# Kernel optimization log

Measured on AMD Instinct MI355X. Metric: run time of the kernel, lower is better.

The kernel has to match this reference:

```python
import jax, jax.numpy as jnp
import numpy as np

N_FILTRATIONS = 24
TEMPERATURE = 0.15
H1_WEIGHT = 0.5
LAMBDA_TOPO = 0.1


def setup_inputs() -> dict:
    key = jax.random.key(0)
    embeddings = jax.random.normal(key, (4096, 512), dtype=jnp.float32)
    return {"embeddings": embeddings, "step": 0}


def _landscape_loss(embeddings):
    N = embeddings.shape[0]
    emb = embeddings.astype(jnp.float32)
    # pairwise euclidean distances (torch.cdist p=2), safe sqrt for grad at 0
    sq = jnp.sum(emb * emb, axis=1)
    d2 = sq[:, None] + sq[None, :] - 2.0 * (emb @ emb.T)
    d2 = jnp.maximum(d2, 0.0)
    pos = d2 > 1e-12
    dist = jnp.where(pos, jnp.sqrt(jnp.where(pos, d2, 1.0)), 0.0)
    eye = jnp.eye(N, dtype=jnp.float32)
    dist = dist + eye * 1e9  # [N, N], diag pushed to 'infinity'
    off = dist < 1e8
    # thresholds come from .item() in torch -> no grad through them
    d_min = jax.lax.stop_gradient(jnp.min(jnp.where(off, dist, jnp.inf)))
    d_max = jax.lax.stop_gradient(
        jnp.maximum(jnp.max(jnp.where(off, dist, -jnp.inf)), d_min + 1e-4))
    thresholds = jnp.linspace(d_min, d_max, N_FILTRATIONS)

    one_minus_eye = 1.0 - eye

    def step_fn(carry, thresh):
        adj = jax.nn.sigmoid((thresh - dist) / TEMPERATURE) * one_minus_eye
        deg = jnp.clip(jnp.sum(adj, axis=-1), 1e-6, None)
        n_isolated = jnp.sum((deg < 0.5).astype(jnp.float32))  # H0 proxy
        n_edges_soft = jnp.sum(adj) / 2.0
        n_excess = jax.nn.relu(n_edges_soft - (N - 1)) / N  # H1 proxy
        return carry, (n_isolated, n_excess)

    _, (h0, h1) = jax.lax.scan(step_fn, None, thresholds)
    h0_loss = jnp.mean(h0[-8:])
    h1_loss = jnp.mean(h1)
    total = h0_loss + H1_WEIGHT * h1_loss
    return total * LAMBDA_TOPO


def reference(embeddings, step) -> jnp.ndarray:
    # warmup_steps = 0, so the warmup skip branch never triggers;
    # N == max_points, so no subsampling.
    return _landscape_loss(embeddings)
```

## Files before the change

### kernel.cpp

```cpp
#include <hip/hip_runtime.h>
#include <stdint.h>

typedef float f32x4 __attribute__((ext_vector_type(4)));
typedef short s16x8 __attribute__((ext_vector_type(8)));
typedef unsigned short us4 __attribute__((ext_vector_type(4)));

#define NPTS 4096
#define DDIM 512
#define NF   24
#define NBLK 32
#define NB   2048

#define OFF_SQ  4194304
#define OFF_MM  4210688
#define OFF_DEG 4210752
#define OFF_D   4603968
#define OFF_H   38158400ULL
#define WS_A    54935616ULL

typedef __attribute__((address_space(1))) void gvoid;
typedef __attribute__((address_space(3))) void svoid;
#define GLD16(gp, lp) __builtin_amdgcn_global_load_lds((gvoid*)(gp), (svoid*)(lp), 16, 0, 0)

static __device__ __forceinline__ ushort f2h(float x) {
    _Float16 h = (_Float16)x;
    return __builtin_bit_cast(unsigned short, h);
}
static __device__ __forceinline__ float h2f(ushort u) {
    return (float)__builtin_bit_cast(_Float16, u);
}

__global__ __launch_bounds__(256) void k_init(float* __restrict__ deg,
                                              unsigned* __restrict__ mm) {
    int i = blockIdx.x * 256 + threadIdx.x;
    if (i < NPTS * NF) deg[i] = 0.0f;
    if (i == 0) { mm[0] = 0x7F7FFFFFu; mm[1] = 0u; }
}

__global__ __launch_bounds__(256) void k_convert(const float* __restrict__ in,
                                                 ushort* __restrict__ Eb,
                                                 float* __restrict__ sq,
                                                 float* __restrict__ acc32,
                                                 unsigned* __restrict__ mm) {
    if (blockIdx.x == 0) {
        if (threadIdx.x < 32) acc32[threadIdx.x] = 0.0f;
        else if (threadIdx.x == 32) mm[0] = 0x7F7FFFFFu;
        else if (threadIdx.x == 33) mm[1] = 0u;
    }
    const int w = threadIdx.x >> 6, lane = threadIdx.x & 63;
    const int row = blockIdx.x * 4 + w;
    const float* src = in + (size_t)row * DDIM + lane * 8;
    float4 a = ((const float4*)src)[0];
    float4 b = ((const float4*)src)[1];
    float v[8] = {a.x, a.y, a.z, a.w, b.x, b.y, b.z, b.w};
    unsigned u[8];
    float ss = 0.0f;
#pragma unroll
    for (int i = 0; i < 8; ++i) {
        ss += v[i] * v[i];
        unsigned bits = __float_as_uint(v[i]);
        u[i] = (bits + 0x7FFFu + ((bits >> 16) & 1u)) >> 16;
    }
    uint4 pk;
    pk.x = u[0] | (u[1] << 16);
    pk.y = u[2] | (u[3] << 16);
    pk.z = u[4] | (u[5] << 16);
    pk.w = u[6] | (u[7] << 16);
    *(uint4*)(Eb + (size_t)row * DDIM + lane * 8) = pk;
#pragma unroll
    for (int s = 1; s < 64; s <<= 1) ss += __shfl_xor(ss, s);
    if (lane == 0) sq[row] = ss;
}

__global__ __launch_bounds__(256) void k_gram_v3u(const ushort* __restrict__ Eb,
                                                  const float* __restrict__ sq,
                                                  unsigned* __restrict__ mm,
                                                  ushort* __restrict__ D2h) {
    __shared__ __align__(16) ushort SM[17408];
    __shared__ float sqr[128], sqc[128], red[8];
    char* SMb = (char*)SM;
    const int tid = threadIdx.x;
    const int w = tid >> 6, lane = tid & 63, g = lane >> 4, l15 = lane & 15;
    const int wr = w >> 1, wc = w & 1;

    int bid = blockIdx.x, rb = 0, pre = 0;
    while (pre + (NBLK - rb) <= bid) { pre += NBLK - rb; ++rb; }
    const int cb = rb + (bid - pre);

    if (tid < 128) sqr[tid] = sq[rb * 128 + tid];
    else           sqc[tid - 128] = sq[cb * 128 + (tid - 128)];

    f32x4 acc[4][4];
#pragma unroll
    for (int i = 0; i < 4; ++i)
#pragma unroll
        for (int j = 0; j < 4; ++j) acc[i][j] = (f32x4){0.f, 0.f, 0.f, 0.f};

    const int lrow = lane >> 2, lch = lane & 3;

#define STAGE(buf, kk)                                                          \
    {                                                                           \
        const int k0_ = (kk) * 32;                                              \
        _Pragma("unroll")                                                       \
        for (int i_ = 0; i_ < 2; ++i_) {                                        \
            const int r_  = w * 32 + i_ * 16 + lrow;                            \
            const int ch_ = lch ^ ((r_ >> 1) & 3);                              \
            GLD16(Eb + (size_t)(rb * 128 + r_) * DDIM + k0_ + ch_ * 8,          \
                  SMb + (buf) * 8192 + (w * 32 + i_ * 16) * 64);                \
            GLD16(Eb + (size_t)(cb * 128 + r_) * DDIM + k0_ + ch_ * 8,          \
                  SMb + 16384 + (buf) * 8192 + (w * 32 + i_ * 16) * 64);        \
        }                                                                       \
    }

    STAGE(0, 0);
    int cur = 0;
#pragma unroll 1
    for (int kk = 0; kk < 16; ++kk) {
        __syncthreads();
        if (kk < 15) STAGE(cur ^ 1, kk + 1);
        s16x8 rf[4], cf[4];
#pragma unroll
        for (int i = 0; i < 4; ++i) {
            const int r = wr * 64 + i * 16 + l15;
            rf[i] = *(const s16x8*)(SMb + cur * 8192 + r * 64 + ((g ^ ((r >> 1) & 3)) * 16));
        }
#pragma unroll
        for (int j = 0; j < 4; ++j) {
            const int r = wc * 64 + j * 16 + l15;
            cf[j] = *(const s16x8*)(SMb + 16384 + cur * 8192 + r * 64 + ((g ^ ((r >> 1) & 3)) * 16));
        }
#pragma unroll
        for (int i = 0; i < 4; ++i)
#pragma unroll
            for (int j = 0; j < 4; ++j)
                acc[i][j] = __builtin_amdgcn_mfma_f32_16x16x32_bf16(cf[j], rf[i], acc[i][j], 0, 0, 0);
        cur ^= 1;
    }
    __syncthreads();

    ushort* T = SM;
    float mn = 3.4e38f, mx = 0.0f;
#pragma unroll
    for (int i = 0; i < 4; ++i) {
        const int lr = wr * 64 + i * 16 + l15;
        const int trow = rb * 128 + lr;
        const float srv = sqr[lr];
#pragma unroll
        for (int j = 0; j < 4; ++j) {
            const int c0 = wc * 64 + j * 16 + g * 4;
            const int tc0 = cb * 128 + c0;
            ushort h[4];
#pragma unroll
            for (int m = 0; m < 4; ++m) {
                float d2 = srv + sqc[c0 + m] - 2.0f * acc[i][j][m];
                d2 = fmaxf(d2, 0.0f);
                bool diag = (tc0 + m == trow);
                mn = diag ? mn : fminf(mn, d2);
                mx = diag ? mx : fmaxf(mx, d2);
                h[m] = f2h(diag ? 6.0e4f : d2);
            }
            us4 pk4 = {h[0], h[1], h[2], h[3]};
            *(us4*)(T + lr * 136 + c0) = pk4;
        }
    }
#pragma unroll
    for (int s = 1; s < 64; s <<= 1) {
        mn = fminf(mn, __shfl_xor(mn, s));
        mx = fmaxf(mx, __shfl_xor(mx, s));
    }
    if (lane == 0) { red[w] = mn; red[4 + w] = mx; }
    __syncthreads();
    if (tid == 0) {
        mn = fminf(fminf(red[0], red[1]), fminf(red[2], red[3]));
        mx = fmaxf(fmaxf(red[4], red[5]), fmaxf(red[6], red[7]));
        atomicMin(&mm[0], __float_as_uint(mn));
        atomicMax(&mm[1], __float_as_uint(mx));
    }
#pragma unroll
    for (int j = 0; j < 8; ++j) {
        const int c = j * 256 + tid;
        const int row = c >> 4, col8 = (c & 15) * 8;
        uint4 v = *(const uint4*)(T + row * 136 + col8);
        *(uint4*)(D2h + (size_t)(rb * 128 + row) * NPTS + cb * 128 + col8) = v;
    }
    if (rb != cb) {
        __syncthreads();
#pragma unroll
        for (int i = 0; i < 4; ++i) {
            const int lr = wr * 64 + i * 16 + l15;
            const float srv = sqr[lr];
#pragma unroll
            for (int j = 0; j < 4; ++j) {
                const int c0 = wc * 64 + j * 16 + g * 4;
#pragma unroll
                for (int m = 0; m < 4; ++m) {
                    float d2 = srv + sqc[c0 + m] - 2.0f * acc[i][j][m];
                    d2 = fmaxf(d2, 0.0f);
                    T[(c0 + m) * 136 + lr] = f2h(d2);
                }
            }
        }
        __syncthreads();
#pragma unroll
        for (int j2 = 0; j2 < 8; ++j2) {
            const int c = j2 * 256 + tid;
            const int row = c >> 4, col8 = (c & 15) * 8;
            uint4 v = *(const uint4*)(T + row * 136 + col8);
            *(uint4*)(D2h + (size_t)(cb * 128 + row) * NPTS + rb * 128 + col8) = v;
        }
    }
}

__global__ __launch_bounds__(256) void k_hist4(const ushort* __restrict__ D2h,
                                               const unsigned* __restrict__ mm,
                                               ushort* __restrict__ H) {
    __shared__ unsigned Hs[4][NB + 4];
    const int tid = threadIdx.x, w = tid >> 6, lane = tid & 63;
    const int row0 = blockIdx.x * 4;
    const int row = row0 + w;
    for (int i = tid; i < 4 * (NB + 4); i += 256) ((unsigned*)Hs)[i] = 0u;
    const float d2min = __uint_as_float(mm[0]);
    const float d2max = __uint_as_float(mm[1]);
    const float sc = (float)NB / fmaxf(d2max - d2min, 1e-6f);
    __syncthreads();
    const uint4* Dv = (const uint4*)(D2h + (size_t)row * NPTS);
    unsigned* hr = Hs[w];
#pragma unroll
    for (int it = 0; it < 8; ++it) {
        uint4 pk = Dv[it * 64 + lane];
        unsigned pw[4] = {pk.x, pk.y, pk.z, pk.w};
#pragma unroll
        for (int i = 0; i < 4; ++i) {
            float a = h2f((ushort)(pw[i] & 0xFFFFu));
            float b = h2f((ushort)(pw[i] >> 16));
            if (a < 3.0e4f) {
                int ba = (int)fminf(fmaxf((a - d2min) * sc, 0.0f), (float)(NB - 1));
                atomicAdd(&hr[ba], 1u);
            }
            if (b < 3.0e4f) {
                int bb = (int)fminf(fmaxf((b - d2min) * sc, 0.0f), (float)(NB - 1));
                atomicAdd(&hr[bb], 1u);
            }
        }
    }
    __syncthreads();
    unsigned* Ho = (unsigned*)(H + (size_t)row0 * NB);
    for (int i = tid; i < 4 * (NB / 2); i += 256) {
        const int r = i >> 10, pw_ = i & 1023;
        unsigned lo = Hs[r][2 * pw_], hi = Hs[r][2 * pw_ + 1];
        Ho[r * (NB / 2) + pw_] = (lo & 0xFFFFu) | (hi << 16);
    }
}

__global__ __launch_bounds__(512) void k_dot(const ushort* __restrict__ H,
                                             const unsigned* __restrict__ mm,
                                             float* __restrict__ acc32) {
    __shared__ float Wl[4][NB];
    __shared__ float degb[8][NF];
    const int tid = threadIdx.x;
    const int wid = tid >> 6, lane = tid & 63;
    const int row = blockIdx.x * 8 + wid;

    const float d2min = __uint_as_float(mm[0]);
    const float d2max = __uint_as_float(mm[1]);
    const float bw    = fmaxf(d2max - d2min, 1e-6f) / (float)NB;
    const float d_min = d2min > 1e-12f ? sqrtf(d2min) : 0.0f;
    const float d_mx  = d2max > 1e-12f ? sqrtf(d2max) : 0.0f;
    const float d_max = fmaxf(d_mx, d_min + 1e-4f);
    const float stp   = (d_max - d_min) / 23.0f;
    const float S2L   = (1.0f / 0.15f) * 1.44269504f;
    const float Ds2   = stp * S2L;
    const float R     = exp2f(-Ds2);
    const float LIM   = 1073741824.0f;

    float hv[32];
    const ushort* Hr = H + (size_t)row * NB;
#pragma unroll
    for (int j = 0; j < 8; ++j) {
        uint2 pk = *(const uint2*)(Hr + j * 256 + lane * 4);
        hv[j * 4 + 0] = (float)(pk.x & 0xFFFFu);
        hv[j * 4 + 1] = (float)(pk.x >> 16);
        hv[j * 4 + 2] = (float)(pk.y & 0xFFFFu);
        hv[j * 4 + 3] = (float)(pk.y >> 16);
    }

    float e4[4];
#pragma unroll
    for (int q = 0; q < 4; ++q) {
        const int b = tid * 4 + q;
        const float d2c = d2min + ((float)b + 0.5f) * bw;
        const float db = sqrtf(fmaxf(d2c, 0.0f));
        e4[q] = exp2f(fminf((db - d_min) * S2L, 125.0f));
    }

#pragma unroll 1
    for (int ph = 0; ph < 6; ++ph) {
        __syncthreads();
#pragma unroll
        for (int k = 0; k < 4; ++k) {
            f32x4 sg;
#pragma unroll
            for (int q = 0; q < 4; ++q) {
                sg[q] = __builtin_amdgcn_rcpf(1.0f + fminf(e4[q], LIM));
                e4[q] *= R;
            }
            *(f32x4*)(&Wl[k][tid * 4]) = sg;
        }
        __syncthreads();
        float dacc[4];
#pragma unroll
        for (int k = 0; k < 4; ++k) {
            const float* Wr = &Wl[k][0];
            float s = 0.0f;
#pragma unroll
            for (int j = 0; j < 8; ++j) {
                const f32x4 wv = *(const f32x4*)(Wr + j * 256 + lane * 4);
                s += hv[j*4+0]*wv[0] + hv[j*4+1]*wv[1] + hv[j*4+2]*wv[2] + hv[j*4+3]*wv[3];
            }
            dacc[k] = s;
        }
#pragma unroll
        for (int k = 0; k < 4; ++k)
#pragma unroll
            for (int o = 1; o < 64; o <<= 1) dacc[k] += __shfl_xor(dacc[k], o);
        if (lane == 0) {
#pragma unroll
            for (int k = 0; k < 4; ++k) degb[wid][ph * 4 + k] = dacc[k];
        }
    }
    __syncthreads();
    if (tid < NF) {
        float s = 0.0f;
#pragma unroll
        for (int r = 0; r < 8; ++r) s += degb[r][tid];
        atomicAdd(&acc32[tid], s);
    } else if (tid < 32) {
        const int k = 16 + (tid - NF);
        float c = 0.0f;
#pragma unroll
        for (int r = 0; r < 8; ++r) c += (degb[r][k] < 0.5f) ? 1.0f : 0.0f;
        atomicAdd(&acc32[tid], c);
    }
}

__global__ __launch_bounds__(64) void k_final2(const float* __restrict__ acc32,
                                               float* __restrict__ out) {
    if (threadIdx.x == 0) {
        float h1 = 0.0f;
#pragma unroll
        for (int k = 0; k < NF; ++k)
            h1 += fmaxf(acc32[k] * 0.5f - (float)(NPTS - 1), 0.0f) * (1.0f / (float)NPTS);
        float h0 = 0.0f;
#pragma unroll
        for (int k = 0; k < 8; ++k) h0 += acc32[NF + k];
        out[0] = (h0 * 0.125f + 0.5f * (h1 * (1.0f / 24.0f))) * 0.1f;
    }
}

__device__ __forceinline__ void gram_tile(const ushort* __restrict__ Eb, int rb, int cb,
                                          ushort* As, ushort* Bs, f32x4 acc[2][8]) {
    const int tid = threadIdx.x;
    const int w = tid >> 6, lane = tid & 63, g = lane >> 4, l15 = lane & 15;
#pragma unroll 1
    for (int kk = 0; kk < DDIM / 32; ++kk) {
        const int k0 = kk * 32;
        __syncthreads();
#pragma unroll
        for (int it = 0; it < 2; ++it) {
            int li  = it * 256 + tid;
            int row = li >> 2, ch = li & 3;
            uint4 va = *(const uint4*)(Eb + (size_t)(rb * 128 + row) * DDIM + k0 + ch * 8);
            uint4 vb = *(const uint4*)(Eb + (size_t)(cb * 128 + row) * DDIM + k0 + ch * 8);
            *(uint4*)(As + row * 32 + ch * 8) = va;
            *(uint4*)(Bs + row * 32 + ch * 8) = vb;
        }
        __syncthreads();
        s16x8 rf0 = *(const s16x8*)(As + (w * 32 + 0 * 16 + l15) * 32 + g * 8);
        s16x8 rf1 = *(const s16x8*)(As + (w * 32 + 1 * 16 + l15) * 32 + g * 8);
#pragma unroll
        for (int bj = 0; bj < 8; ++bj) {
            s16x8 cf = *(const s16x8*)(Bs + (bj * 16 + l15) * 32 + g * 8);
            acc[0][bj] = __builtin_amdgcn_mfma_f32_16x16x32_bf16(cf, rf0, acc[0][bj], 0, 0, 0);
            acc[1][bj] = __builtin_amdgcn_mfma_f32_16x16x32_bf16(cf, rf1, acc[1][bj], 0, 0, 0);
        }
    }
}

__global__ __launch_bounds__(256) void k_minmax(const ushort* __restrict__ Eb,
                                                const float* __restrict__ sq,
                                                unsigned* __restrict__ mm) {
    const int rb = blockIdx.y, cb = blockIdx.x;
    if (cb < rb) return;
    __shared__ ushort As[128 * 32], Bs[128 * 32];
    __shared__ float sqr[128], sqc[128];
    __shared__ float red[8];
    const int tid = threadIdx.x;
    if (tid < 128) sqr[tid] = sq[rb * 128 + tid];
    else           sqc[tid - 128] = sq[cb * 128 + (tid - 128)];
    f32x4 acc[2][8];
#pragma unroll
    for (int bi = 0; bi < 2; ++bi)
#pragma unroll
        for (int bj = 0; bj < 8; ++bj) acc[bi][bj] = (f32x4){0.f, 0.f, 0.f, 0.f};
    gram_tile(Eb, rb, cb, As, Bs, acc);
    const int w = tid >> 6, lane = tid & 63, g = lane >> 4, l15 = lane & 15;
    const float sr0 = sqr[w * 32 + l15], sr1 = sqr[w * 32 + 16 + l15];
    float mn = 3.4e38f, mx = 0.0f;
#pragma unroll
    for (int bi = 0; bi < 2; ++bi)
#pragma unroll
        for (int bj = 0; bj < 8; ++bj)
#pragma unroll
            for (int m = 0; m < 4; ++m) {
                int tr = w * 32 + bi * 16 + l15;
                int tc = bj * 16 + g * 4 + m;
                float d2 = (bi ? sr1 : sr0) + sqc[tc] - 2.0f * acc[bi][bj][m];
                d2 = fmaxf(d2, 0.0f);
                bool diag = (rb == cb) && (tr == tc);
                mn = diag ? mn : fminf(mn, d2);
                mx = diag ? mx : fmaxf(mx, d2);
            }
#pragma unroll
    for (int s = 1; s < 64; s <<= 1) {
        mn = fminf(mn, __shfl_xor(mn, s));
        mx = fmaxf(mx, __shfl_xor(mx, s));
    }
    if (lane == 0) { red[w] = mn; red[4 + w] = mx; }
    __syncthreads();
    if (tid == 0) {
        mn = fminf(fminf(red[0], red[1]), fminf(red[2], red[3]));
        mx = fmaxf(fmaxf(red[4], red[5]), fmaxf(red[6], red[7]));
        atomicMin(&mm[0], __float_as_uint(mn));
        atomicMax(&mm[1], __float_as_uint(mx));
    }
}

__global__ __launch_bounds__(256) void k_accum2(const ushort* __restrict__ Eb,
                                                const float* __restrict__ sq,
                                                const unsigned* __restrict__ mm,
                                                float* __restrict__ deg) {
    const int rb = blockIdx.y, cb = blockIdx.x;
    __shared__ ushort As[128 * 32], Bs[128 * 32];
    __shared__ float sqr[128], sqc[128];
    __shared__ float degr[128][NF];
    const int tid = threadIdx.x;
    if (tid < 128) sqr[tid] = sq[rb * 128 + tid];
    else           sqc[tid - 128] = sq[cb * 128 + (tid - 128)];
    for (int i = tid; i < 128 * NF; i += 256) ((float*)degr)[i] = 0.0f;
    f32x4 acc[2][8];
#pragma unroll
    for (int bi = 0; bi < 2; ++bi)
#pragma unroll
        for (int bj = 0; bj < 8; ++bj) acc[bi][bj] = (f32x4){0.f, 0.f, 0.f, 0.f};
    gram_tile(Eb, rb, cb, As, Bs, acc);
    const int w = tid >> 6, lane = tid & 63, g = lane >> 4, l15 = lane & 15;

    const float dmin2 = __uint_as_float(mm[0]);
    const float dmax2 = __uint_as_float(mm[1]);
    const float d_min = dmin2 > 1e-12f ? sqrtf(dmin2) : 0.0f;
    const float d_mx  = dmax2 > 1e-12f ? sqrtf(dmax2) : 0.0f;
    const float d_max = fmaxf(d_mx, d_min + 1e-4f);
    const float stp   = (d_max - d_min) / 23.0f;
    const float S2L   = (1.0f / 0.15f) * 1.44269504f;
    const float Ds2   = stp * S2L;
    const float R     = exp2f(-Ds2);
    const float LIM   = 1073741824.0f;
    const float ECAP  = 125.0f;

    const float sr0 = sqr[w * 32 + l15], sr1 = sqr[w * 32 + 16 + l15];
    f32x4 ee[2][8];
#pragma unroll
    for (int bi = 0; bi < 2; ++bi)
#pragma unroll
        for (int bj = 0; bj < 8; ++bj)
#pragma unroll
            for (int m = 0; m < 4; ++m) {
                int tr = w * 32 + bi * 16 + l15;
                int tc = bj * 16 + g * 4 + m;
                float d2 = (bi ? sr1 : sr0) + sqc[tc] - 2.0f * acc[bi][bj][m];
                d2 = fmaxf(d2, 0.0f);
                float d = d2 > 1e-12f ? sqrtf(d2) : 0.0f;
                if (rb == cb && tr == tc) d = 1e9f;
                ee[bi][bj][m] = exp2f(fminf((d - d_min) * S2L, ECAP));
            }

#pragma unroll 1
    for (int t = 0; t < NF; ++t) {
        float rs0 = 0.0f, rs1 = 0.0f;
#pragma unroll
        for (int bj = 0; bj < 8; ++bj) {
            {
                f32x4 q = ee[0][bj];
                float A  = 1.0f + fminf(q.x, LIM), B  = 1.0f + fminf(q.y, LIM);
                float Cq = 1.0f + fminf(q.z, LIM), Dq = 1.0f + fminf(q.w, LIM);
                float sAB = A + B,  sCD = Cq + Dq;
                float pAB = A * B,  pCD = Cq * Dq;
                rs0 += (sAB * pCD + sCD * pAB) * __builtin_amdgcn_rcpf(pAB * pCD);
                ee[0][bj] = q * R;
            }
            {
                f32x4 q = ee[1][bj];
                float A  = 1.0f + fminf(q.x, LIM), B  = 1.0f + fminf(q.y, LIM);
                float Cq = 1.0f + fminf(q.z, LIM), Dq = 1.0f + fminf(q.w, LIM);
                float sAB = A + B,  sCD = Cq + Dq;
                float pAB = A * B,  pCD = Cq * Dq;
                rs1 += (sAB * pCD + sCD * pAB) * __builtin_amdgcn_rcpf(pAB * pCD);
                ee[1][bj] = q * R;
            }
        }
        rs0 += __shfl_xor(rs0, 16); rs0 += __shfl_xor(rs0, 32);
        rs1 += __shfl_xor(rs1, 16); rs1 += __shfl_xor(rs1, 32);
        if (g == 0) {
            degr[w * 32 + l15][t]      += rs0;
            degr[w * 32 + 16 + l15][t] += rs1;
        }
    }
    __syncthreads();
    for (int i = tid; i < 128 * NF; i += 256) {
        int r = i / NF, t = i % NF;
        atomicAdd(&deg[(size_t)(rb * 128 + r) * NF + t], degr[r][t]);
    }
}

__global__ __launch_bounds__(256) void k_final(const float* __restrict__ deg,
                                               float* __restrict__ out) {
    const int tid = threadIdx.x;
    float s[NF], cnt[8];
#pragma unroll
    for (int t = 0; t < NF; ++t) s[t] = 0.0f;
#pragma unroll
    for (int k = 0; k < 8; ++k) cnt[k] = 0.0f;
    for (int i = tid; i < NPTS; i += 256) {
        const float* row = deg + (size_t)i * NF;
#pragma unroll
        for (int t = 0; t < NF; ++t) {
            float v = row[t];
            s[t] += v;
            if (t >= 16) cnt[t - 16] += (v < 0.5f) ? 1.0f : 0.0f;
        }
    }
#pragma unroll
    for (int t = 0; t < NF; ++t)
#pragma unroll
        for (int o = 1; o < 64; o <<= 1) s[t] += __shfl_xor(s[t], o);
#pragma unroll
    for (int k = 0; k < 8; ++k)
#pragma unroll
        for (int o = 1; o < 64; o <<= 1) cnt[k] += __shfl_xor(cnt[k], o);
    __shared__ float red[4][32];
    const int w = tid >> 6, lane = tid & 63;
    if (lane == 0) {
#pragma unroll
        for (int t = 0; t < NF; ++t) red[w][t] = s[t];
#pragma unroll
        for (int k = 0; k < 8; ++k) red[w][NF + k] = cnt[k];
    }
    __syncthreads();
    if (tid == 0) {
        float h0 = 0.0f, h1 = 0.0f;
#pragma unroll
        for (int t = 0; t < NF; ++t) {
            float S = red[0][t] + red[1][t] + red[2][t] + red[3][t];
            float edges = S * 0.5f;
            h1 += fmaxf(edges - (float)(NPTS - 1), 0.0f) / (float)NPTS;
        }
#pragma unroll
        for (int k = 0; k < 8; ++k)
            h0 += red[0][NF + k] + red[1][NF + k] + red[2][NF + k] + red[3][NF + k];
        h0 *= (1.0f / 8.0f);
        h1 *= (1.0f / 24.0f);
        out[0] = (h0 + 0.5f * h1) * 0.1f;
    }
}

extern "C" void kernel_launch(void* const* d_in, const int* in_sizes, int n_in,
                              void* d_out, int out_size, void* d_ws, size_t ws_size,
                              hipStream_t stream) {
    (void)in_sizes; (void)n_in; (void)out_size;
    const float* emb = (const float*)d_in[0];
    uint8_t* ws = (uint8_t*)d_ws;
    ushort*   Eb  = (ushort*)(ws);
    float*    sqv = (float*)(ws + OFF_SQ);
    unsigned* mm  = (unsigned*)(ws + OFF_MM);
    float*    deg = (float*)(ws + OFF_DEG);
    ushort*   D2h = (ushort*)(ws + OFF_D);
    ushort*   H   = (ushort*)(ws + OFF_H);
    float*    out = (float*)d_out;
    const bool bigws = (ws_size >= WS_A);

    if (bigws) {
        k_convert <<<dim3(NPTS / 4),              dim3(256), 0, stream>>>(emb, Eb, sqv, deg, mm);
        k_gram_v3u<<<dim3(NBLK * (NBLK + 1) / 2), dim3(256), 0, stream>>>(Eb, sqv, mm, D2h);
        k_hist4   <<<dim3(NPTS / 4),              dim3(256), 0, stream>>>(D2h, mm, H);
        k_dot     <<<dim3(NPTS / 8),              dim3(512), 0, stream>>>(H, mm, deg);
        k_final2  <<<dim3(1),                     dim3(64),  0, stream>>>(deg, out);
    } else {
        k_init   <<<dim3(384),      dim3(256), 0, stream>>>(deg, mm);
        k_convert<<<dim3(NPTS / 4), dim3(256), 0, stream>>>(emb, Eb, sqv, deg, mm);
        k_minmax <<<dim3(32, 32),   dim3(256), 0, stream>>>(Eb, sqv, mm);
        k_accum2 <<<dim3(32, 32),   dim3(256), 0, stream>>>(Eb, sqv, mm, deg);
        k_final  <<<dim3(1),        dim3(256), 0, stream>>>(deg, out);
    }
}
```

Before: 85.48 us.

## Triple-buffer gram kernel LDS stages with explicit vmcnt waits

Replaces the double-buffered K loop in the bf16 gram kernel with a three-stage LDS ring buffer. Two tiles are prefetched ahead, and precise s_waitcnt vmcnt counts let loads stay in flight across iterations instead of draining at every barrier. This hides more global-load latency behind the MFMA work. In exchange it uses more shared memory per block, which may lower occupancy, and the hand-counted waits must match the number of issued loads.

```diff
diff --git a/kernel.cpp b/kernel.cpp
--- a/kernel.cpp
+++ b/kernel.cpp
@@ -76,7 +76,7 @@
                                                   const float* __restrict__ sq,
                                                   unsigned* __restrict__ mm,
                                                   ushort* __restrict__ D2h) {
-    __shared__ __align__(16) ushort SM[17408];
+    __shared__ __align__(16) ushort SM[24576];
     __shared__ float sqr[128], sqc[128], red[8];
     char* SMb = (char*)SM;
     const int tid = threadIdx.x;
@@ -108,34 +108,50 @@
             GLD16(Eb + (size_t)(rb * 128 + r_) * DDIM + k0_ + ch_ * 8,          \
                   SMb + (buf) * 8192 + (w * 32 + i_ * 16) * 64);                \
             GLD16(Eb + (size_t)(cb * 128 + r_) * DDIM + k0_ + ch_ * 8,          \
-                  SMb + 16384 + (buf) * 8192 + (w * 32 + i_ * 16) * 64);        \
+                  SMb + 24576 + (buf) * 8192 + (w * 32 + i_ * 16) * 64);        \
         }                                                                       \
     }
 
+#define KSTEP(WAITN, kk, DOSTAGE)                                               \
+    {                                                                           \
+        asm volatile("s_waitcnt vmcnt(" #WAITN ")" ::: "memory");               \
+        __builtin_amdgcn_s_barrier();                                           \
+        __builtin_amdgcn_sched_barrier(0);                                      \
+        const char* Ac = SMb + bcur * 8192;                                     \
+        const char* Bc = SMb + 24576 + bcur * 8192;                             \
+        s16x8 rf[4], cf[4];                                                     \
+        _Pragma("unroll")                                                       \
+        for (int i = 0; i < 4; ++i) {                                           \
+            const int r = wr * 64 + i * 16 + l15;                               \
+            rf[i] = *(const s16x8*)(Ac + r * 64 + ((g ^ ((r >> 1) & 3)) * 16)); \
+        }                                                                       \
+        _Pragma("unroll")                                                       \
+        for (int j = 0; j < 4; ++j) {                                           \
+            const int r = wc * 64 + j * 16 + l15;                               \
+            cf[j] = *(const s16x8*)(Bc + r * 64 + ((g ^ ((r >> 1) & 3)) * 16)); \
+        }                                                                       \
+        _Pragma("unroll")                                                       \
+        for (int i = 0; i < 4; ++i)                                             \
+            _Pragma("unroll")                                                   \
+            for (int j = 0; j < 4; ++j)                                         \
+                acc[i][j] = __builtin_amdgcn_mfma_f32_16x16x32_bf16(            \
+                    cf[j], rf[i], acc[i][j], 0, 0, 0);                          \
+        asm volatile("s_waitcnt lgkmcnt(0)" ::: "memory");                      \
+        __builtin_amdgcn_s_barrier();                                           \
+        __builtin_amdgcn_sched_barrier(0);                                      \
+        if (DOSTAGE) { STAGE(bcur, (kk) + 3); }                                 \
+        bcur = (bcur == 2) ? 0 : bcur + 1;                                      \
+    }
+
     STAGE(0, 0);
-    int cur = 0;
+    STAGE(1, 1);
+    STAGE(2, 2);
+    int bcur = 0;
 #pragma unroll 1
-    for (int kk = 0; kk < 16; ++kk) {
-        __syncthreads();
-        if (kk < 15) STAGE(cur ^ 1, kk + 1);
-        s16x8 rf[4], cf[4];
-#pragma unroll
-        for (int i = 0; i < 4; ++i) {
-            const int r = wr * 64 + i * 16 + l15;
-            rf[i] = *(const s16x8*)(SMb + cur * 8192 + r * 64 + ((g ^ ((r >> 1) & 3)) * 16));
-        }
-#pragma unroll
-        for (int j = 0; j < 4; ++j) {
-            const int r = wc * 64 + j * 16 + l15;
-            cf[j] = *(const s16x8*)(SMb + 16384 + cur * 8192 + r * 64 + ((g ^ ((r >> 1) & 3)) * 16));
-        }
-#pragma unroll
-        for (int i = 0; i < 4; ++i)
-#pragma unroll
-            for (int j = 0; j < 4; ++j)
-                acc[i][j] = __builtin_amdgcn_mfma_f32_16x16x32_bf16(cf[j], rf[i], acc[i][j], 0, 0, 0);
-        cur ^= 1;
-    }
+    for (int kk = 0; kk < 13; ++kk) KSTEP(8, kk, 1);
+    KSTEP(8, 13, 0);
+    KSTEP(4, 14, 0);
+    KSTEP(0, 15, 0);
     __syncthreads();
 
     ushort* T = SM;
```

Measured after the change: 89.37 us. +4.5%, slower.

## Deepen Gram GEMM K-tile to 64 and remap block order for XCD locality

Applied to the files above, without the earlier changes.

The Gram kernel now stages 64-wide K slices instead of 32, halving the number of loop iterations and barriers. It uses a 128-byte-row LDS layout with an XOR-8 swizzle and does two MFMA sub-steps per stage. It also permutes block IDs so that consecutive triangle tiles go to the same XCD (stride 8, 66 blocks each), aiming for better L2 reuse of row panels. LDS use doubles to 64KB plus extras, which may lower occupancy per CU.

```diff
diff --git a/kernel.cpp b/kernel.cpp
--- a/kernel.cpp
+++ b/kernel.cpp
@@ -72,18 +72,19 @@
     if (lane == 0) sq[row] = ss;
 }
 
-__global__ __launch_bounds__(256) void k_gram_v3u(const ushort* __restrict__ Eb,
-                                                  const float* __restrict__ sq,
-                                                  unsigned* __restrict__ mm,
-                                                  ushort* __restrict__ D2h) {
-    __shared__ __align__(16) ushort SM[17408];
+__global__ __launch_bounds__(256) void k_gram_bk64(const ushort* __restrict__ Eb,
+                                                   const float* __restrict__ sq,
+                                                   unsigned* __restrict__ mm,
+                                                   ushort* __restrict__ D2h) {
+    __shared__ __align__(16) ushort SM[32768];
     __shared__ float sqr[128], sqc[128], red[8];
     char* SMb = (char*)SM;
     const int tid = threadIdx.x;
     const int w = tid >> 6, lane = tid & 63, g = lane >> 4, l15 = lane & 15;
     const int wr = w >> 1, wc = w & 1;
 
-    int bid = blockIdx.x, rb = 0, pre = 0;
+    int bid = (blockIdx.x & 7) * 66 + (blockIdx.x >> 3);
+    int rb = 0, pre = 0;
     while (pre + (NBLK - rb) <= bid) { pre += NBLK - rb; ++rb; }
     const int cb = rb + (bid - pre);
 
@@ -96,44 +97,52 @@
 #pragma unroll
         for (int j = 0; j < 4; ++j) acc[i][j] = (f32x4){0.f, 0.f, 0.f, 0.f};
 
-    const int lrow = lane >> 2, lch = lane & 3;
-
-#define STAGE(buf, kk)                                                          \
+    const int srow_off = lane >> 3, slch = lane & 7;
+
+#define STAGE64(buf, kk)                                                        \
     {                                                                           \
-        const int k0_ = (kk) * 32;                                              \
+        const int k0_ = (kk) * 64;                                              \
         _Pragma("unroll")                                                       \
-        for (int i_ = 0; i_ < 2; ++i_) {                                        \
-            const int r_  = w * 32 + i_ * 16 + lrow;                            \
-            const int ch_ = lch ^ ((r_ >> 1) & 3);                              \
+        for (int i_ = 0; i_ < 4; ++i_) {                                        \
+            const int r_  = w * 32 + i_ * 8 + srow_off;                         \
+            const int ch_ = slch ^ (r_ & 7);                                    \
             GLD16(Eb + (size_t)(rb * 128 + r_) * DDIM + k0_ + ch_ * 8,          \
-                  SMb + (buf) * 8192 + (w * 32 + i_ * 16) * 64);                \
+                  SMb + (buf) * 16384 + (w * 32 + i_ * 8) * 128);               \
             GLD16(Eb + (size_t)(cb * 128 + r_) * DDIM + k0_ + ch_ * 8,          \
-                  SMb + 16384 + (buf) * 8192 + (w * 32 + i_ * 16) * 64);        \
+                  SMb + 32768 + (buf) * 16384 + (w * 32 + i_ * 8) * 128);       \
         }                                                                       \
     }
 
-    STAGE(0, 0);
+    STAGE64(0, 0);
     int cur = 0;
 #pragma unroll 1
-    for (int kk = 0; kk < 16; ++kk) {
+    for (int kk = 0; kk < 8; ++kk) {
         __syncthreads();
-        if (kk < 15) STAGE(cur ^ 1, kk + 1);
-        s16x8 rf[4], cf[4];
-#pragma unroll
-        for (int i = 0; i < 4; ++i) {
-            const int r = wr * 64 + i * 16 + l15;
-            rf[i] = *(const s16x8*)(SMb + cur * 8192 + r * 64 + ((g ^ ((r >> 1) & 3)) * 16));
-        }
-#pragma unroll
-        for (int j = 0; j < 4; ++j) {
-            const int r = wc * 64 + j * 16 + l15;
-            cf[j] = *(const s16x8*)(SMb + 16384 + cur * 8192 + r * 64 + ((g ^ ((r >> 1) & 3)) * 16));
-        }
-#pragma unroll
-        for (int i = 0; i < 4; ++i)
-#pragma unroll
-            for (int j = 0; j < 4; ++j)
-                acc[i][j] = __builtin_amdgcn_mfma_f32_16x16x32_bf16(cf[j], rf[i], acc[i][j], 0, 0, 0);
+        if (kk < 7) STAGE64(cur ^ 1, kk + 1);
+        const char* Ac = SMb + cur * 16384;
+        const char* Bc = SMb + 32768 + cur * 16384;
+#pragma unroll
+        for (int ks = 0; ks < 2; ++ks) {
+            s16x8 rf[4], cf[4];
+#pragma unroll
+            for (int i = 0; i < 4; ++i) {
+                const int r = wr * 64 + i * 16 + l15;
+                const int slot = (ks * 4 + g) ^ (r & 7);
+                rf[i] = *(const s16x8*)(Ac + r * 128 + slot * 16);
+            }
+#pragma unroll
+            for (int j = 0; j < 4; ++j) {
+                const int r = wc * 64 + j * 16 + l15;
+                const int slot = (ks * 4 + g) ^ (r & 7);
+                cf[j] = *(const s16x8*)(Bc + r * 128 + slot * 16);
+            }
+#pragma unroll
+            for (int i = 0; i < 4; ++i)
+#pragma unroll
+                for (int j = 0; j < 4; ++j)
+                    acc[i][j] = __builtin_amdgcn_mfma_f32_16x16x32_bf16(
+                        cf[j], rf[i], acc[i][j], 0, 0, 0);
+        }
         cur ^= 1;
     }
     __syncthreads();
@@ -590,7 +599,7 @@
 
     if (bigws) {
         k_convert <<<dim3(NPTS / 4),              dim3(256), 0, stream>>>(emb, Eb, sqv, deg, mm);
-        k_gram_v3u<<<dim3(NBLK * (NBLK + 1) / 2), dim3(256), 0, stream>>>(Eb, sqv, mm, D2h);
+        k_gram_bk64<<<dim3(NBLK * (NBLK + 1) / 2), dim3(256), 0, stream>>>(Eb, sqv, mm, D2h);
         k_hist4   <<<dim3(NPTS / 4),              dim3(256), 0, stream>>>(D2h, mm, H);
         k_dot     <<<dim3(NPTS / 8),              dim3(512), 0, stream>>>(H, mm, deg);
         k_final2  <<<dim3(1),                     dim3(64),  0, stream>>>(deg, out);
```

Measured after the change: 83.09 us. -2.8%, faster.

## Load gram-kernel MFMA fragments directly from global memory, skipping LDS staging

Applied to the files above, without the earlier changes.

The Gram-matrix kernel no longer stages tiles of the bf16 embeddings into LDS with global_load_lds. Each lane now loads its MFMA fragments straight from global memory into registers, double-buffered across k-steps, and the per-step barriers are gone. The LDS buffer is kept only for the epilogue transpose. Block IDs are also remapped with a stride-66 interleave, likely to spread the triangular tiles across XCDs. This trades LDS traffic and synchronisation for redundant global and L2 loads, since each row fragment is fetched by two waves, and for higher register pressure.

```diff
diff --git a/kernel.cpp b/kernel.cpp
--- a/kernel.cpp
+++ b/kernel.cpp
@@ -17,10 +17,6 @@
 #define OFF_D   4603968
 #define OFF_H   38158400ULL
 #define WS_A    54935616ULL
-
-typedef __attribute__((address_space(1))) void gvoid;
-typedef __attribute__((address_space(3))) void svoid;
-#define GLD16(gp, lp) __builtin_amdgcn_global_load_lds((gvoid*)(gp), (svoid*)(lp), 16, 0, 0)
 
 static __device__ __forceinline__ ushort f2h(float x) {
     _Float16 h = (_Float16)x;
@@ -72,18 +68,18 @@
     if (lane == 0) sq[row] = ss;
 }
 
-__global__ __launch_bounds__(256) void k_gram_v3u(const ushort* __restrict__ Eb,
-                                                  const float* __restrict__ sq,
-                                                  unsigned* __restrict__ mm,
-                                                  ushort* __restrict__ D2h) {
-    __shared__ __align__(16) ushort SM[17408];
+__global__ __launch_bounds__(256) void k_gram_nolds(const ushort* __restrict__ Eb,
+                                                    const float* __restrict__ sq,
+                                                    unsigned* __restrict__ mm,
+                                                    ushort* __restrict__ D2h) {
+    __shared__ __align__(16) ushort T[128 * 136];
     __shared__ float sqr[128], sqc[128], red[8];
-    char* SMb = (char*)SM;
     const int tid = threadIdx.x;
     const int w = tid >> 6, lane = tid & 63, g = lane >> 4, l15 = lane & 15;
     const int wr = w >> 1, wc = w & 1;
 
-    int bid = blockIdx.x, rb = 0, pre = 0;
+    int bid = (blockIdx.x & 7) * 66 + (blockIdx.x >> 3);
+    int rb = 0, pre = 0;
     while (pre + (NBLK - rb) <= bid) { pre += NBLK - rb; ++rb; }
     const int cb = rb + (bid - pre);
 
@@ -96,49 +92,39 @@
 #pragma unroll
         for (int j = 0; j < 4; ++j) acc[i][j] = (f32x4){0.f, 0.f, 0.f, 0.f};
 
-    const int lrow = lane >> 2, lch = lane & 3;
-
-#define STAGE(buf, kk)                                                          \
-    {                                                                           \
-        const int k0_ = (kk) * 32;                                              \
-        _Pragma("unroll")                                                       \
-        for (int i_ = 0; i_ < 2; ++i_) {                                        \
-            const int r_  = w * 32 + i_ * 16 + lrow;                            \
-            const int ch_ = lch ^ ((r_ >> 1) & 3);                              \
-            GLD16(Eb + (size_t)(rb * 128 + r_) * DDIM + k0_ + ch_ * 8,          \
-                  SMb + (buf) * 8192 + (w * 32 + i_ * 16) * 64);                \
-            GLD16(Eb + (size_t)(cb * 128 + r_) * DDIM + k0_ + ch_ * 8,          \
-                  SMb + 16384 + (buf) * 8192 + (w * 32 + i_ * 16) * 64);        \
-        }                                                                       \
-    }
-
-    STAGE(0, 0);
-    int cur = 0;
-#pragma unroll 1
+    const ushort* rfp[4];
+    const ushort* cfp[4];
+#pragma unroll
+    for (int i = 0; i < 4; ++i) {
+        rfp[i] = Eb + (size_t)(rb * 128 + wr * 64 + i * 16 + l15) * DDIM + g * 8;
+        cfp[i] = Eb + (size_t)(cb * 128 + wc * 64 + i * 16 + l15) * DDIM + g * 8;
+    }
+
+    s16x8 fr[2][4], fc[2][4];
+#pragma unroll
+    for (int i = 0; i < 4; ++i) {
+        fr[0][i] = *(const s16x8*)(rfp[i]);
+        fc[0][i] = *(const s16x8*)(cfp[i]);
+    }
+#pragma unroll
     for (int kk = 0; kk < 16; ++kk) {
-        __syncthreads();
-        if (kk < 15) STAGE(cur ^ 1, kk + 1);
-        s16x8 rf[4], cf[4];
-#pragma unroll
-        for (int i = 0; i < 4; ++i) {
-            const int r = wr * 64 + i * 16 + l15;
-            rf[i] = *(const s16x8*)(SMb + cur * 8192 + r * 64 + ((g ^ ((r >> 1) & 3)) * 16));
-        }
-#pragma unroll
-        for (int j = 0; j < 4; ++j) {
-            const int r = wc * 64 + j * 16 + l15;
-            cf[j] = *(const s16x8*)(SMb + 16384 + cur * 8192 + r * 64 + ((g ^ ((r >> 1) & 3)) * 16));
+        const int cur = kk & 1, nxt = cur ^ 1;
+        if (kk < 15) {
+#pragma unroll
+            for (int i = 0; i < 4; ++i) {
+                fr[nxt][i] = *(const s16x8*)(rfp[i] + (kk + 1) * 32);
+                fc[nxt][i] = *(const s16x8*)(cfp[i] + (kk + 1) * 32);
+            }
         }
 #pragma unroll
         for (int i = 0; i < 4; ++i)
 #pragma unroll
             for (int j = 0; j < 4; ++j)
-                acc[i][j] = __builtin_amdgcn_mfma_f32_16x16x32_bf16(cf[j], rf[i], acc[i][j], 0, 0, 0);
-        cur ^= 1;
-    }
-    __syncthreads();
-
-    ushort* T = SM;
+                acc[i][j] = __builtin_amdgcn_mfma_f32_16x16x32_bf16(
+                    fc[cur][j], fr[cur][i], acc[i][j], 0, 0, 0);
+    }
+    __syncthreads();
+
     float mn = 3.4e38f, mx = 0.0f;
 #pragma unroll
     for (int i = 0; i < 4; ++i) {
@@ -589,11 +575,11 @@
     const bool bigws = (ws_size >= WS_A);
 
     if (bigws) {
-        k_convert <<<dim3(NPTS / 4),              dim3(256), 0, stream>>>(emb, Eb, sqv, deg, mm);
-        k_gram_v3u<<<dim3(NBLK * (NBLK + 1) / 2), dim3(256), 0, stream>>>(Eb, sqv, mm, D2h);
-        k_hist4   <<<dim3(NPTS / 4),              dim3(256), 0, stream>>>(D2h, mm, H);
-        k_dot     <<<dim3(NPTS / 8),              dim3(512), 0, stream>>>(H, mm, deg);
-        k_final2  <<<dim3(1),                     dim3(64),  0, stream>>>(deg, out);
+        k_convert  <<<dim3(NPTS / 4),               dim3(256), 0, stream>>>(emb, Eb, sqv, deg, mm);
+        k_gram_nolds<<<dim3(NBLK * (NBLK + 1) / 2), dim3(256), 0, stream>>>(Eb, sqv, mm, D2h);
+        k_hist4    <<<dim3(NPTS / 4),               dim3(256), 0, stream>>>(D2h, mm, H);
+        k_dot      <<<dim3(NPTS / 8),               dim3(512), 0, stream>>>(H, mm, deg);
+        k_final2   <<<dim3(1),                      dim3(64),  0, stream>>>(deg, out);
     } else {
         k_init   <<<dim3(384),      dim3(256), 0, stream>>>(deg, mm);
         k_convert<<<dim3(NPTS / 4), dim3(256), 0, stream>>>(emb, Eb, sqv, deg, mm);
```

Result: slower. 102.0 us (+19.3%).
